# Performance work log

Measured on AMD Instinct MI355X. Metric: run time of the kernel, lower is better.

## Reference

```python
import jax, jax.numpy as jnp
import numpy as np

NUM_GENES = 4384
D_MODEL = 128


def setup_inputs() -> dict:
    key = jax.random.key(0)
    ks = jax.random.split(key, 8)
    B = 8
    return {
        "mutation_input": jax.random.normal(ks[0], (B, NUM_GENES, 4), dtype=jnp.float32),
        "external_V": jax.random.normal(ks[1], (NUM_GENES, D_MODEL), dtype=jnp.float32),
        "W_in": jax.random.normal(ks[2], (4, D_MODEL), dtype=jnp.float32) * 0.5,
        "b_in": jnp.zeros((D_MODEL,), dtype=jnp.float32),
        "key_param": jax.random.normal(ks[3], (NUM_GENES, D_MODEL), dtype=jnp.float32),
        "W1": jax.random.normal(ks[4], (D_MODEL, 64), dtype=jnp.float32) * (1.0 / np.sqrt(D_MODEL)),
        "b1": jnp.zeros((64,), dtype=jnp.float32),
        "W2": jax.random.normal(ks[5], (64, 26), dtype=jnp.float32) * 0.125,
        "b2": jnp.zeros((26,), dtype=jnp.float32),
    }


def reference(mutation_input, external_V, W_in, b_in, key_param, W1, b1, W2, b2):
    # Q: [B, G, D]
    Q = jnp.einsum("bgf,fd->bgd", mutation_input, W_in) + b_in
    scale = 1.0 / jnp.sqrt(jnp.asarray(Q.shape[-1], Q.dtype))
    # scores: [B, G, G] -- full matrix as in the original module
    scores = jnp.einsum("bqd,kd->bqk", Q, key_param) * scale
    attn = jax.nn.softmax(scores, axis=-1)
    # attention output: [B, G, D]
    attn_out = jnp.einsum("bqk,kd->bqd", attn, external_V)
    mean_out = attn_out.mean(axis=1)  # [B, D]
    h = jax.nn.gelu(mean_out @ W1 + b1, approximate=False)
    out = h @ W2 + b2  # [B, 26]
    return out
```

## Files before the change

kernel.cpp:

```cpp
#include <hip/hip_runtime.h>
#include <hip/hip_bf16.h>

#define NUM_GENES 4384
#define GPAD 4608
#define DM 128
#define ROWB 256
#define LDS_STRIDE 272
#define NTILES 137
#define RB_BLOCKS 18
#define NCHUNK 6
#define TPC 23
#define TOTAL_BLK 864u

typedef __attribute__((ext_vector_type(8))) short short8;
typedef __attribute__((ext_vector_type(16))) float floatx16;

#if defined(__has_builtin)
#  if __has_builtin(__builtin_amdgcn_exp2f)
#    define FAST_EXP2(x) __builtin_amdgcn_exp2f(x)
#  endif
#endif
#ifndef FAST_EXP2
#  define FAST_EXP2(x) exp2f(x)
#endif

static __device__ __forceinline__ short bf16bits(float x) {
    __hip_bfloat16 h = __float2bfloat16(x);
    return *(short*)&h;
}

__global__ __launch_bounds__(256)
void prep_all(const float* __restrict__ mut, const float* __restrict__ W_in,
              const float* __restrict__ b_in, const float* __restrict__ key,
              __hip_bfloat16* __restrict__ Qb, __hip_bfloat16* __restrict__ Kb,
              float* __restrict__ l, float* __restrict__ meanbuf,
              unsigned* __restrict__ donecnt) {
    int bx = blockIdx.x, t = threadIdx.x;
    if (bx < 2304) {
        int i = bx * 256 + t;
        int d0 = (i & 15) * 8;
        int g = (i >> 4) % GPAD;
        int b = i / (GPAD * 16);
        short8 o;
        if (g < NUM_GENES) {
            const float4 mv = *(const float4*)(mut + ((size_t)b * NUM_GENES + g) * 4);
            const float sc = 0.08838834764831845f * 1.4426950408889634f;
#pragma unroll
            for (int j = 0; j < 8; ++j) {
                int d = d0 + j;
                float v = b_in[d] + mv.x * W_in[d] + mv.y * W_in[128 + d]
                                  + mv.z * W_in[256 + d] + mv.w * W_in[384 + d];
                o[j] = bf16bits(v * sc);
            }
        } else {
#pragma unroll
            for (int j = 0; j < 8; ++j) o[j] = 0;
        }
        *(short8*)((short*)Qb + (size_t)i * 8) = o;
    } else if (bx < 2592) {
        int i = (bx - 2304) * 256 + t;
        int g = i >> 4;
        short8 o;
        if (g < NUM_GENES) {
            const float4 k0 = *(const float4*)(key + (size_t)i * 8);
            const float4 k1 = *(const float4*)(key + (size_t)i * 8 + 4);
            o[0] = bf16bits(k0.x); o[1] = bf16bits(k0.y);
            o[2] = bf16bits(k0.z); o[3] = bf16bits(k0.w);
            o[4] = bf16bits(k1.x); o[5] = bf16bits(k1.y);
            o[6] = bf16bits(k1.z); o[7] = bf16bits(k1.w);
        } else {
#pragma unroll
            for (int j = 0; j < 8; ++j) o[j] = 0;
        }
        *(short8*)((short*)Kb + (size_t)i * 8) = o;
    } else {
        int i = (bx - 2592) * 256 + t;
        float4 z = {0.f, 0.f, 0.f, 0.f};
        *(float4*)(l + (size_t)i * 8) = z;
        *(float4*)(l + (size_t)i * 8 + 4) = z;
        if (bx == 2592) {
            if (t < 128) {
                *(float4*)(meanbuf + t * 8) = z;
                *(float4*)(meanbuf + t * 8 + 4) = z;
            }
            if (t == 0) *donecnt = 0u;
        }
    }
}

template <bool PB>
__global__ __launch_bounds__(256)
void phase_kernel(const __hip_bfloat16* __restrict__ Qb,
                  const __hip_bfloat16* __restrict__ Kb,
                  const float* __restrict__ lsum,
                  const float* __restrict__ V,
                  const float* __restrict__ W1, const float* __restrict__ b1,
                  const float* __restrict__ W2, const float* __restrict__ b2,
                  float* __restrict__ outv,
                  float* __restrict__ final_out,
                  unsigned* __restrict__ donecnt) {
    __shared__ __align__(16) char tile[2][32 * LDS_STRIDE];

    int rb    = blockIdx.x;
    int chunk = blockIdx.y;
    int b     = blockIdx.z;

    const char* resident = (const char*)(PB ? Kb : (Qb + (size_t)b * GPAD * DM));
    const char* stream   = (const char*)(PB ? (Qb + (size_t)b * GPAD * DM) : Kb);

    int t = threadIdx.x;
    int lane = t & 63, wid = t >> 6;
    int m = lane & 31, half = lane >> 5;

    short8 afrag[2][8];
#pragma unroll
    for (int g = 0; g < 2; ++g) {
        const char* arow = resident + (size_t)(rb * 256 + wid * 64 + g * 32 + m) * ROWB;
#pragma unroll
        for (int dsl = 0; dsl < 8; ++dsl)
            afrag[g][dsl] = *(const short8*)(arow + dsl * 32 + half * 16);
    }

    float lacc[2][16];
#pragma unroll
    for (int g = 0; g < 2; ++g)
#pragma unroll
        for (int r = 0; r < 16; ++r) lacc[g][r] = 0.f;

    int t0 = chunk * TPC;
    int t1 = min(NTILES, t0 + TPC);
    int sr = t >> 3, sc = t & 7;
    int soff = sr * LDS_STRIDE + sc * 32;

    {
        const char* src = stream + (size_t)(t0 * 32 + sr) * ROWB + sc * 32;
        float4 v0 = *(const float4*)src;
        float4 v1 = *(const float4*)(src + 16);
        *(float4*)(tile[0] + soff) = v0;
        *(float4*)(tile[0] + soff + 16) = v1;
    }

    int p = 0;
    for (int kt = t0; kt < t1; ++kt) {
        bool more = (kt + 1 < t1);
        float4 v0, v1;
        if (more) {
            const char* s2 = stream + (size_t)((kt + 1) * 32 + sr) * ROWB + sc * 32;
            v0 = *(const float4*)s2;
            v1 = *(const float4*)(s2 + 16);
        }
        __syncthreads();

        floatx16 acc0, acc1;
#pragma unroll
        for (int r = 0; r < 16; ++r) { acc0[r] = 0.f; acc1[r] = 0.f; }
#pragma unroll
        for (int dsl = 0; dsl < 8; ++dsl) {
            short8 bfrag = *(const short8*)(tile[p] + m * LDS_STRIDE + dsl * 32 + half * 16);
            acc0 = __builtin_amdgcn_mfma_f32_32x32x16_bf16(afrag[0][dsl], bfrag, acc0, 0, 0, 0);
            acc1 = __builtin_amdgcn_mfma_f32_32x32x16_bf16(afrag[1][dsl], bfrag, acc1, 0, 0, 0);
        }

        if (more) {
            *(float4*)(tile[p ^ 1] + soff) = v0;
            *(float4*)(tile[p ^ 1] + soff + 16) = v1;
        }

        if (PB) {
            float scl = __builtin_amdgcn_rcpf(lsum[b * GPAD + kt * 32 + m]);
#pragma unroll
            for (int r = 0; r < 16; ++r) {
                lacc[0][r] = fmaf(FAST_EXP2(acc0[r]), scl, lacc[0][r]);
                lacc[1][r] = fmaf(FAST_EXP2(acc1[r]), scl, lacc[1][r]);
            }
        } else {
#pragma unroll
            for (int r = 0; r < 16; ++r) {
                lacc[0][r] += FAST_EXP2(acc0[r]);
                lacc[1][r] += FAST_EXP2(acc1[r]);
            }
        }
        p ^= 1;
    }

#pragma unroll
    for (int off = 1; off <= 16; off <<= 1)
#pragma unroll
        for (int g = 0; g < 2; ++g)
#pragma unroll
            for (int r = 0; r < 16; ++r)
                lacc[g][r] += __shfl_xor(lacc[g][r], off, 64);

    if constexpr (!PB) {
        if (m == 0) {
#pragma unroll
            for (int g = 0; g < 2; ++g) {
                float* ob = outv + b * GPAD + rb * 256 + wid * 64 + g * 32 + 4 * half;
#pragma unroll
                for (int r = 0; r < 16; ++r)
                    atomicAdd(ob + (r & 3) + 8 * (r >> 2), lacc[g][r]);
            }
        }
    } else {
        __shared__ float sw[256];
        __shared__ int slast;
        __syncthreads();
        if (m == 0) {
#pragma unroll
            for (int g = 0; g < 2; ++g) {
                int base = wid * 64 + g * 32 + 4 * half;
#pragma unroll
                for (int r = 0; r < 16; ++r) {
                    int rl = base + (r & 3) + 8 * (r >> 2);
                    sw[rl] = (rb * 256 + rl < NUM_GENES) ? lacc[g][r] : 0.f;
                }
            }
        }
        __syncthreads();
        {
            int d = t & 127, hf = t >> 7;
            int gbase = rb * 256 + hf * 128;
            int cnt = NUM_GENES - gbase;
            if (cnt > 128) cnt = 128;
            if (cnt > 0) {
                const float* swp = sw + hf * 128;
                const float* Vp = V + (size_t)gbase * 128 + d;
                float a0 = 0.f, a1 = 0.f;
                int k = 0;
                for (; k + 1 < cnt; k += 2) {
                    a0 += swp[k] * Vp[(size_t)k * 128];
                    a1 += swp[k + 1] * Vp[(size_t)(k + 1) * 128];
                }
                if (k < cnt) a0 += swp[k] * Vp[(size_t)k * 128];
                atomicAdd(outv + b * 128 + d, a0 + a1);
            }
        }
        __syncthreads();
        if (t == 0) {
            __threadfence();
            slast = (atomicAdd(donecnt, 1u) == TOTAL_BLK - 1u) ? 1 : 0;
        }
        __syncthreads();
        if (slast) {
            __threadfence();
            __shared__ float smean[1024];
            __shared__ float shh[512];
            for (int i = t; i < 1024; i += 256)
                smean[i] = __hip_atomic_load((float*)outv + i, __ATOMIC_RELAXED,
                                             __HIP_MEMORY_SCOPE_AGENT);
            __syncthreads();
            for (int pair = t; pair < 512; pair += 256) {
                int bb = pair >> 6, h = pair & 63;
                const float* mb = smean + bb * 128;
                float s = b1[h];
                for (int d = 0; d < 128; ++d)
                    s += (mb[d] * (1.0f / 4384.0f)) * W1[d * 64 + h];
                shh[pair] = 0.5f * s * (1.0f + erff(s * 0.70710678118654752f));
            }
            __syncthreads();
            if (t < 208) {
                int bb = t / 26, j = t % 26;
                const float* hp = shh + bb * 64;
                float o = b2[j];
                for (int k = 0; k < 64; ++k) o += hp[k] * W2[k * 26 + j];
                final_out[bb * 26 + j] = o;
            }
        }
    }
}

extern "C" void kernel_launch(void* const* d_in, const int* in_sizes, int n_in,
                              void* d_out, int out_size, void* d_ws, size_t ws_size,
                              hipStream_t stream) {
    const float* mut  = (const float*)d_in[0];
    const float* V    = (const float*)d_in[1];
    const float* W_in = (const float*)d_in[2];
    const float* b_in = (const float*)d_in[3];
    const float* key  = (const float*)d_in[4];
    const float* W1   = (const float*)d_in[5];
    const float* b1   = (const float*)d_in[6];
    const float* W2   = (const float*)d_in[7];
    const float* b2   = (const float*)d_in[8];
    float* out = (float*)d_out;

    char* ws = (char*)d_ws;
    __hip_bfloat16* Qb = (__hip_bfloat16*)(ws);
    __hip_bfloat16* Kb = (__hip_bfloat16*)(ws + 9437184);
    float* lbuf        = (float*)(ws + 10616832);
    float* meanbuf     = (float*)(ws + 10764288);
    unsigned* donecnt  = (unsigned*)(ws + 10768384);

    prep_all<<<2610, 256, 0, stream>>>(mut, W_in, b_in, key, Qb, Kb, lbuf, meanbuf, donecnt);

    dim3 grid(RB_BLOCKS, NCHUNK, 8);
    phase_kernel<false><<<grid, 256, 0, stream>>>(
        Qb, Kb, lbuf, V, nullptr, nullptr, nullptr, nullptr, lbuf, nullptr, nullptr);
    phase_kernel<true><<<grid, 256, 0, stream>>>(
        Qb, Kb, lbuf, V, W1, b1, W2, b2, meanbuf, out, donecnt);
}
```

Baseline: 233.9 us.

## Fuse both attention phases into one persistent kernel with grid-wide barriers

Merges the two phase kernels into a single kernel of 864 blocks that spin-wait on global atomic counters as grid barriers between the softmax-denominator pass, the weighting pass, a distributed V reduction and the final MLP. The V·weight product now runs as a separate stage spread over all blocks, writing per-slice partials that 8 blocks then reduce. The aim is to drop a kernel launch and the serial last-block tail. In exchange it depends on all 864 blocks being co-resident, which the launch bounds of 4 blocks per CU are meant to allow. It also reuses the Qb workspace region for the partial sums.

After: 581.2 us. 149% more time.

```diff
diff --git a/kernel.cpp b/kernel.cpp
--- a/kernel.cpp
+++ b/kernel.cpp
@@ -33,8 +33,8 @@
 void prep_all(const float* __restrict__ mut, const float* __restrict__ W_in,
               const float* __restrict__ b_in, const float* __restrict__ key,
               __hip_bfloat16* __restrict__ Qb, __hip_bfloat16* __restrict__ Kb,
-              float* __restrict__ l, float* __restrict__ meanbuf,
-              unsigned* __restrict__ donecnt) {
+              float* __restrict__ l, float* __restrict__ w,
+              unsigned* __restrict__ cnt) {
     int bx = blockIdx.x, t = threadIdx.x;
     if (bx < 2304) {
         int i = bx * 256 + t;
@@ -78,37 +78,37 @@
         float4 z = {0.f, 0.f, 0.f, 0.f};
         *(float4*)(l + (size_t)i * 8) = z;
         *(float4*)(l + (size_t)i * 8 + 4) = z;
-        if (bx == 2592) {
-            if (t < 128) {
-                *(float4*)(meanbuf + t * 8) = z;
-                *(float4*)(meanbuf + t * 8 + 4) = z;
-            }
-            if (t == 0) *donecnt = 0u;
-        }
-    }
+        *(float4*)(w + (size_t)i * 8) = z;
+        *(float4*)(w + (size_t)i * 8 + 4) = z;
+        if (bx == 2592 && t < 4) cnt[t] = 0u;
+    }
+}
+
+static __device__ __forceinline__ void gsync(unsigned* c, int t) {
+    __syncthreads();
+    if (t == 0) {
+        __hip_atomic_fetch_add(c, 1u, __ATOMIC_RELEASE, __HIP_MEMORY_SCOPE_AGENT);
+        int guard = 0;
+        while (__hip_atomic_load(c, __ATOMIC_RELAXED, __HIP_MEMORY_SCOPE_AGENT) < TOTAL_BLK
+               && guard < (1 << 24)) {
+            __builtin_amdgcn_s_sleep(1);
+            ++guard;
+        }
+        (void)__hip_atomic_load(c, __ATOMIC_ACQUIRE, __HIP_MEMORY_SCOPE_AGENT);
+    }
+    __syncthreads();
 }
 
 template <bool PB>
-__global__ __launch_bounds__(256)
-void phase_kernel(const __hip_bfloat16* __restrict__ Qb,
-                  const __hip_bfloat16* __restrict__ Kb,
-                  const float* __restrict__ lsum,
-                  const float* __restrict__ V,
-                  const float* __restrict__ W1, const float* __restrict__ b1,
-                  const float* __restrict__ W2, const float* __restrict__ b2,
-                  float* __restrict__ outv,
-                  float* __restrict__ final_out,
-                  unsigned* __restrict__ donecnt) {
-    __shared__ __align__(16) char tile[2][32 * LDS_STRIDE];
-
-    int rb    = blockIdx.x;
-    int chunk = blockIdx.y;
-    int b     = blockIdx.z;
+static __device__ __forceinline__
+void phase_body(int rb, int chunk, int b, int t,
+                const __hip_bfloat16* Qb, const __hip_bfloat16* Kb,
+                const float* lsum, float* outv, char* tileraw) {
+    char (*tile)[32 * LDS_STRIDE] = (char (*)[32 * LDS_STRIDE])tileraw;
 
     const char* resident = (const char*)(PB ? Kb : (Qb + (size_t)b * GPAD * DM));
     const char* stream   = (const char*)(PB ? (Qb + (size_t)b * GPAD * DM) : Kb);
 
-    int t = threadIdx.x;
     int lane = t & 63, wid = t >> 6;
     int m = lane & 31, half = lane >> 5;
 
@@ -167,7 +167,9 @@
         }
 
         if (PB) {
-            float scl = __builtin_amdgcn_rcpf(lsum[b * GPAD + kt * 32 + m]);
+            float lv = __hip_atomic_load(lsum + b * GPAD + kt * 32 + m,
+                                         __ATOMIC_RELAXED, __HIP_MEMORY_SCOPE_AGENT);
+            float scl = __builtin_amdgcn_rcpf(lv);
 #pragma unroll
             for (int r = 0; r < 16; ++r) {
                 lacc[0][r] = fmaf(FAST_EXP2(acc0[r]), scl, lacc[0][r]);
@@ -191,80 +193,92 @@
             for (int r = 0; r < 16; ++r)
                 lacc[g][r] += __shfl_xor(lacc[g][r], off, 64);
 
-    if constexpr (!PB) {
-        if (m == 0) {
-#pragma unroll
-            for (int g = 0; g < 2; ++g) {
-                float* ob = outv + b * GPAD + rb * 256 + wid * 64 + g * 32 + 4 * half;
-#pragma unroll
-                for (int r = 0; r < 16; ++r)
-                    atomicAdd(ob + (r & 3) + 8 * (r >> 2), lacc[g][r]);
-            }
-        }
-    } else {
-        __shared__ float sw[256];
-        __shared__ int slast;
-        __syncthreads();
-        if (m == 0) {
-#pragma unroll
-            for (int g = 0; g < 2; ++g) {
-                int base = wid * 64 + g * 32 + 4 * half;
-#pragma unroll
-                for (int r = 0; r < 16; ++r) {
-                    int rl = base + (r & 3) + 8 * (r >> 2);
-                    sw[rl] = (rb * 256 + rl < NUM_GENES) ? lacc[g][r] : 0.f;
-                }
-            }
-        }
-        __syncthreads();
-        {
-            int d = t & 127, hf = t >> 7;
-            int gbase = rb * 256 + hf * 128;
-            int cnt = NUM_GENES - gbase;
-            if (cnt > 128) cnt = 128;
-            if (cnt > 0) {
-                const float* swp = sw + hf * 128;
-                const float* Vp = V + (size_t)gbase * 128 + d;
-                float a0 = 0.f, a1 = 0.f;
-                int k = 0;
-                for (; k + 1 < cnt; k += 2) {
-                    a0 += swp[k] * Vp[(size_t)k * 128];
-                    a1 += swp[k + 1] * Vp[(size_t)(k + 1) * 128];
-                }
-                if (k < cnt) a0 += swp[k] * Vp[(size_t)k * 128];
-                atomicAdd(outv + b * 128 + d, a0 + a1);
-            }
-        }
-        __syncthreads();
-        if (t == 0) {
-            __threadfence();
-            slast = (atomicAdd(donecnt, 1u) == TOTAL_BLK - 1u) ? 1 : 0;
-        }
-        __syncthreads();
-        if (slast) {
-            __threadfence();
-            __shared__ float smean[1024];
-            __shared__ float shh[512];
-            for (int i = t; i < 1024; i += 256)
-                smean[i] = __hip_atomic_load((float*)outv + i, __ATOMIC_RELAXED,
-                                             __HIP_MEMORY_SCOPE_AGENT);
-            __syncthreads();
-            for (int pair = t; pair < 512; pair += 256) {
-                int bb = pair >> 6, h = pair & 63;
-                const float* mb = smean + bb * 128;
-                float s = b1[h];
-                for (int d = 0; d < 128; ++d)
-                    s += (mb[d] * (1.0f / 4384.0f)) * W1[d * 64 + h];
-                shh[pair] = 0.5f * s * (1.0f + erff(s * 0.70710678118654752f));
-            }
-            __syncthreads();
-            if (t < 208) {
-                int bb = t / 26, j = t % 26;
-                const float* hp = shh + bb * 64;
-                float o = b2[j];
-                for (int k = 0; k < 64; ++k) o += hp[k] * W2[k * 26 + j];
-                final_out[bb * 26 + j] = o;
-            }
+    if (m == 0) {
+#pragma unroll
+        for (int g = 0; g < 2; ++g) {
+            float* ob = outv + b * GPAD + rb * 256 + wid * 64 + g * 32 + 4 * half;
+#pragma unroll
+            for (int r = 0; r < 16; ++r)
+                atomicAdd(ob + (r & 3) + 8 * (r >> 2), lacc[g][r]);
+        }
+    }
+}
+
+__global__ __launch_bounds__(256, 4)
+void fused_attn(const __hip_bfloat16* __restrict__ Qb,
+                const __hip_bfloat16* __restrict__ Kb,
+                float* __restrict__ lbuf, float* __restrict__ wbuf,
+                float* __restrict__ partial,
+                float* __restrict__ meanbuf,
+                const float* __restrict__ V,
+                const float* __restrict__ W1, const float* __restrict__ b1,
+                const float* __restrict__ W2, const float* __restrict__ b2,
+                float* __restrict__ out, unsigned* __restrict__ cnt) {
+    __shared__ __align__(16) char tile[2 * 32 * LDS_STRIDE];
+    __shared__ float red[256];
+    __shared__ float smean[1024];
+    __shared__ float shh[512];
+
+    int rb = blockIdx.x, chunk = blockIdx.y, b = blockIdx.z;
+    int t = threadIdx.x;
+    int bid = rb + RB_BLOCKS * (chunk + NCHUNK * b);
+
+    phase_body<false>(rb, chunk, b, t, Qb, Kb, nullptr, lbuf, tile);
+    gsync(cnt + 0, t);
+    phase_body<true>(rb, chunk, b, t, Qb, Kb, lbuf, wbuf, tile);
+    gsync(cnt + 1, t);
+
+    {
+        int s = bid % 108, bb = bid / 108;
+        int g0 = s * 43;
+        int cr = NUM_GENES - g0;
+        if (cr > 43) cr = 43;
+        int d = t & 127, hf = t >> 7;
+        float a = 0.f;
+        if (cr > 0) {
+            const float* wp = wbuf + bb * GPAD + g0;
+            const float* Vp = V + (size_t)g0 * 128 + d;
+            for (int k = hf; k < cr; k += 2)
+                a += wp[k] * Vp[(size_t)k * 128];
+        }
+        red[t] = a;
+        __syncthreads();
+        if (t < 128)
+            partial[((size_t)s * 8 + bb) * 128 + t] = red[t] + red[t + 128];
+    }
+    gsync(cnt + 2, t);
+
+    if (bid < 8) {
+        int d = t & 127, hf = t >> 7;
+        float a = 0.f;
+        for (int s = hf; s < 108; s += 2)
+            a += partial[((size_t)s * 8 + bid) * 128 + d];
+        __syncthreads();
+        red[t] = a;
+        __syncthreads();
+        if (t < 128)
+            meanbuf[bid * 128 + t] = (red[t] + red[t + 128]) * (1.0f / 4384.0f);
+    }
+    gsync(cnt + 3, t);
+
+    if (bid == 0) {
+        for (int i = t; i < 1024; i += 256) smean[i] = meanbuf[i];
+        __syncthreads();
+        for (int pair = t; pair < 512; pair += 256) {
+            int bb = pair >> 6, h = pair & 63;
+            const float* mb = smean + bb * 128;
+            float s = b1[h];
+            for (int d = 0; d < 128; ++d)
+                s += mb[d] * W1[d * 64 + h];
+            shh[pair] = 0.5f * s * (1.0f + erff(s * 0.70710678118654752f));
+        }
+        __syncthreads();
+        if (t < 208) {
+            int bb = t / 26, j = t % 26;
+            const float* hp = shh + bb * 64;
+            float o = b2[j];
+            for (int k = 0; k < 64; ++k) o += hp[k] * W2[k * 26 + j];
+            out[bb * 26 + j] = o;
         }
     }
 }
@@ -287,14 +301,14 @@
     __hip_bfloat16* Qb = (__hip_bfloat16*)(ws);
     __hip_bfloat16* Kb = (__hip_bfloat16*)(ws + 9437184);
     float* lbuf        = (float*)(ws + 10616832);
-    float* meanbuf     = (float*)(ws + 10764288);
-    unsigned* donecnt  = (unsigned*)(ws + 10768384);
-
-    prep_all<<<2610, 256, 0, stream>>>(mut, W_in, b_in, key, Qb, Kb, lbuf, meanbuf, donecnt);
+    float* wbuf        = (float*)(ws + 10764288);
+    float* meanbuf     = (float*)(ws + 10911744);
+    unsigned* cnt      = (unsigned*)(ws + 10915840);
+    float* partial     = (float*)(ws);
+
+    prep_all<<<2610, 256, 0, stream>>>(mut, W_in, b_in, key, Qb, Kb, lbuf, wbuf, cnt);
 
     dim3 grid(RB_BLOCKS, NCHUNK, 8);
-    phase_kernel<false><<<grid, 256, 0, stream>>>(
-        Qb, Kb, lbuf, V, nullptr, nullptr, nullptr, nullptr, lbuf, nullptr, nullptr);
-    phase_kernel<true><<<grid, 256, 0, stream>>>(
-        Qb, Kb, lbuf, V, W1, b1, W2, b2, meanbuf, out, donecnt);
-}
+    fused_attn<<<grid, 256, 0, stream>>>(Qb, Kb, lbuf, wbuf, partial, meanbuf,
+                                         V, W1, b1, W2, b2, out, cnt);
+}
```
